# Kernel optimization log

Hardware: AMD Instinct MI355X
Metric: run time of the kernel (lower is better)

Reference implementation:

```python
import jax, jax.numpy as jnp
import numpy as np

# ---- constants mirroring the torch module's fixed config ----
H = W = 128            # raster_settings.image_size
K = 5                  # points_per_pixel
RADIUS = 0.02
R2 = RADIUS * RADIUS
DIST, ELEV = 1.5, 15.0 # look_at_view_transform(1.5, 15, views)
AZIMS = np.array([0.0, 90.0, 180.0, 270.0])
V = len(AZIMS)
ZNEAR, ZFAR = 0.01, 100.0  # FoVOrthographicCameras(znear=0.01), zfar default 100
N_PTS = 4096

def _look_at(dist, elev_deg, azims_deg):
    # pytorch3d camera_position_from_spherical_angles + look_at_rotation
    elev = np.deg2rad(elev_deg)
    az = np.deg2rad(azims_deg)
    C = np.stack([dist*np.cos(elev)*np.sin(az),
                  dist*np.sin(elev)*np.ones_like(az),
                  dist*np.cos(elev)*np.cos(az)], -1)            # [V,3] camera centers
    up = np.array([0.0, 1.0, 0.0])
    z_ax = -C / np.linalg.norm(C, axis=-1, keepdims=True)        # at=(0,0,0)
    x_ax = np.cross(np.broadcast_to(up, z_ax.shape), z_ax)
    x_ax = x_ax / np.linalg.norm(x_ax, axis=-1, keepdims=True)
    y_ax = np.cross(z_ax, x_ax)
    Rm = np.stack([x_ax, y_ax, z_ax], axis=-1)                   # columns = axes; X_view = X @ R + T
    T = -np.einsum('vji,vj->vi', Rm, C)
    return jnp.asarray(Rm, jnp.float32), jnp.asarray(T, jnp.float32)

_R, _T = _look_at(DIST, ELEV, AZIMS)

# pytorch3d NDC pixel centers (flipped: +X left, +Y up), flattened row-major p = yi*W + xi
_xf = 1.0 - (2.0*np.arange(W) + 1.0)/W
_yf = 1.0 - (2.0*np.arange(H) + 1.0)/H
XF = jnp.asarray(np.tile(_xf, H), jnp.float32)    # [H*W]
YF = jnp.asarray(np.repeat(_yf, W), jnp.float32)  # [H*W]


def _forward(pcd, displace, init_colors):
    colors_ = jax.nn.sigmoid(init_colors + displace)                 # [N]
    # world -> view -> NDC (orthographic: x,y pass through; z affine-normalized)
    pv = jnp.einsum('nj,vji->vni', pcd, _R) + _T[:, None, :]          # [V,N,3]
    px, py = pv[..., 0], pv[..., 1]
    pz = (pv[..., 2] - ZNEAR) / (ZFAR - ZNEAR)                        # [V,N]

    # ---- rasterization: per-pixel binning + depth top-K (non-differentiable selection) ----
    pxs, pys, pzs = map(jax.lax.stop_gradient, (px, py, pz))
    def sel(args):
        pxv, pyv, pzv = args                                          # [N] each
        dx = pxv[None, :] - XF[:, None]                               # [HW,N]
        dy = pyv[None, :] - YF[:, None]
        d2 = dx*dx + dy*dy
        score = jnp.where((d2 < R2) & (pzv[None, :] > 0), pzv[None, :], jnp.inf)
        negz, idx = jax.lax.top_k(-score, K)                          # nearest-z first
        return idx, negz
    idx, negz = jax.lax.map(sel, (pxs, pys, pzs))                     # [V,HW,K]
    valid = jnp.isfinite(negz)
    idxc = jnp.clip(idx, 0, pcd.shape[0] - 1)

    # differentiable re-gather of selected splats
    flat = idxc.reshape(V, -1)
    gpx = jnp.take_along_axis(px, flat, axis=1).reshape(idx.shape)    # [V,HW,K]
    gpy = jnp.take_along_axis(py, flat, axis=1).reshape(idx.shape)
    d2s = (gpx - XF[None, :, None])**2 + (gpy - YF[None, :, None])**2

    # ---- alpha compositing: w = 1 - d2/r^2, front-to-back over-composite, black bg ----
    alpha = jnp.where(valid, 1.0 - d2s / R2, 0.0)                     # [V,HW,K]
    feat = colors_[idxc]                                              # grayscale feature per splat
    t = jnp.cumprod(1.0 - alpha, axis=-1)
    t_excl = jnp.concatenate([jnp.ones_like(t[..., :1]), t[..., :-1]], -1)
    pix = jnp.sum(alpha * t_excl * feat, -1)                          # [V,HW]
    images = jnp.broadcast_to(pix[..., None], (V, H*W, 3)).reshape(V, H, W, 3)
    return images, colors_


def setup_inputs() -> dict:
    key = jax.random.key(0)
    k1, k2 = jax.random.split(key)
    pcd = jax.random.uniform(k1, (N_PTS, 3), jnp.float32) - 0.5
    displace = jax.random.normal(k2, (N_PTS,), jnp.float32) * 0.1
    init_colors = jnp.zeros((N_PTS,), jnp.float32)
    return {"pcd": pcd, "displace": displace, "init_colors": init_colors}


def reference(pcd, displace, init_colors):
    return _forward(pcd, displace, init_colors)
```

## Files before the change

kernel.cpp:

```cpp
#include <hip/hip_runtime.h>
#include <hip/hip_bf16.h>
#include <cmath>

#define NPTS  4096
#define HW    16384
#define WIDTH 128
#define NVIEW 4
#define KTOP  5
#define CAP   320

struct AllViews {
    float m[NVIEW][12];
};

__global__ __launch_bounds__(256, 4)
void raster_fused(const float* __restrict__ pcd,
                  const float* __restrict__ displace,
                  const float* __restrict__ init_colors,
                  float* __restrict__ out,
                  float* __restrict__ out_colors,
                  AllViews av) {
    __shared__ float4 buf[CAP];
    __shared__ int cnt;
    __shared__ float mzs[4][64][KTOP];
    __shared__ float mas[4][64][KTOP];
    __shared__ float mcs[4][64][KTOP];

    const int bid  = blockIdx.x;
    const int v    = bid >> 8;
    const int rem  = bid & 255;
    const int y    = rem >> 1;
    const int h    = rem & 1;
    const int tid  = threadIdx.x;
    const int wave = tid >> 6;
    const int lane = tid & 63;
    const float* M = av.m[v];

    if (tid == 0) cnt = 0;
    __syncthreads();

    const float4* __restrict__ pcd4 = (const float4*)pcd;
    const float4* __restrict__ d4   = (const float4*)displace;
    const float4* __restrict__ i4   = (const float4*)init_colors;

    #define PT(N, X0, X1, X2, SC)                                            \
    {                                                                        \
        float x0 = (X0), x1 = (X1), x2 = (X2);                               \
        float py = fmaf(x0, M[3], fmaf(x1, M[4], fmaf(x2, M[5], M[10])));    \
        int b = (int)floorf((1.0f - py) * 64.0f);                            \
        b = min(max(b, 0), 127);                                             \
        if ((b >= y - 1) & (b <= y + 1)) {                                   \
            float px  = fmaf(x0, M[0], fmaf(x1, M[1], fmaf(x2, M[2], M[9]))); \
            float pvz = fmaf(x0, M[6], fmaf(x1, M[7], fmaf(x2, M[8], M[11]))); \
            float pz  = (pvz - 0.01f) * (1.0f / 99.99f);                     \
            int pos = atomicAdd(&cnt, 1);                                    \
            if (pos < CAP) buf[pos] = make_float4(px, py, pz, (SC));         \
        }                                                                    \
        if ((v == 0) & (h == 0) & (((N) >> 5) == y)) out_colors[(N)] = (SC); \
    }

    #pragma unroll 1
    for (int ps = 0; ps < 4; ++ps) {
        float4 A = pcd4[ps * 768 + 3 * tid + 0];
        float4 B = pcd4[ps * 768 + 3 * tid + 1];
        float4 C = pcd4[ps * 768 + 3 * tid + 2];
        float4 D = d4[ps * 256 + tid];
        float4 I = i4[ps * 256 + tid];

        float4 S;
        S.x = 1.0f / (1.0f + expf(-(I.x + D.x)));
        S.y = 1.0f / (1.0f + expf(-(I.y + D.y)));
        S.z = 1.0f / (1.0f + expf(-(I.z + D.z)));
        S.w = 1.0f / (1.0f + expf(-(I.w + D.w)));

        const int n0 = (ps << 10) + (tid << 2);
        PT(n0 + 0, A.x, A.y, A.z, S.x);
        PT(n0 + 1, A.w, B.x, B.y, S.y);
        PT(n0 + 2, B.z, B.w, C.x, S.z);
        PT(n0 + 3, C.y, C.z, C.w, S.w);
    }
    #undef PT
    __syncthreads();

    const int m = min(cnt, CAP);

    const int xi = (h << 6) + lane;
    const float xf = 1.0f - (2.0f * (float)xi + 1.0f) * (1.0f / 128.0f);
    const float yf = 1.0f - (2.0f * (float)y + 1.0f) * (1.0f / 128.0f);

    const float R2f   = (float)(0.02 * 0.02);
    const float invR2 = 1.0f / R2f;

    #define INS(nz, na, nc)                                                 \
    {                                                                       \
        float _z = (nz), _a = (na), _c = (nc);                              \
        _Pragma("unroll")                                                   \
        for (int k = 0; k < KTOP; ++k) {                                    \
            bool sw = _z < zs[k];                                           \
            float oz = zs[k], oa = as_[k], oc = cs[k];                      \
            zs[k]  = sw ? _z : oz;                                          \
            as_[k] = sw ? _a : oa;                                          \
            cs[k]  = sw ? _c : oc;                                          \
            _z = sw ? oz : _z;                                              \
            _a = sw ? oa : _a;                                              \
            _c = sw ? oc : _c;                                              \
        }                                                                   \
    }

    float zs[KTOP], as_[KTOP], cs[KTOP];
    #pragma unroll
    for (int k = 0; k < KTOP; ++k) { zs[k] = 3.0e38f; as_[k] = 0.0f; cs[k] = 0.0f; }

    for (int j = wave; j < m; j += 4) {
        float4 pt = buf[j];
        float dx = pt.x - xf;
        float dy = pt.y - yf;
        float d2 = fmaf(dx, dx, dy * dy);
        if ((d2 < R2f) & (pt.z > 0.0f) & (pt.z < zs[KTOP - 1]))
            INS(pt.z, 1.0f - d2 * invR2, pt.w);
    }

    #pragma unroll
    for (int k = 0; k < KTOP; ++k) {
        mzs[wave][lane][k] = zs[k];
        mas[wave][lane][k] = as_[k];
        mcs[wave][lane][k] = cs[k];
    }
    __syncthreads();

    if (wave == 0) {
        #pragma unroll
        for (int k = 0; k < KTOP; ++k) { zs[k] = 3.0e38f; as_[k] = 0.0f; cs[k] = 0.0f; }
        #pragma unroll
        for (int w = 0; w < 4; ++w) {
            #pragma unroll
            for (int k = 0; k < KTOP; ++k) {
                float nz = mzs[w][lane][k];
                float na = mas[w][lane][k];
                float nc = mcs[w][lane][k];
                if (nz < zs[KTOP - 1]) INS(nz, na, nc);
            }
        }

        float t = 1.0f, pix = 0.0f;
        #pragma unroll
        for (int k = 0; k < KTOP; ++k) {
            pix += as_[k] * t * cs[k];
            t *= (1.0f - as_[k]);
        }

        const int p = v * HW + (y << 7) + xi;
        float* o = out + 3 * (size_t)p;
        o[0] = pix; o[1] = pix; o[2] = pix;
    }
    #undef INS
}

static void compute_views(AllViews* av) {
    const double dist = 1.5;
    const double elev = 15.0 * M_PI / 180.0;
    const double az_deg[NVIEW] = {0.0, 90.0, 180.0, 270.0};
    for (int v = 0; v < NVIEW; ++v) {
        double az = az_deg[v] * M_PI / 180.0;
        double C[3] = { dist * cos(elev) * sin(az),
                        dist * sin(elev),
                        dist * cos(elev) * cos(az) };
        double nC = sqrt(C[0]*C[0] + C[1]*C[1] + C[2]*C[2]);
        double z[3] = { -C[0]/nC, -C[1]/nC, -C[2]/nC };
        double up[3] = { 0.0, 1.0, 0.0 };
        double x[3] = { up[1]*z[2] - up[2]*z[1],
                        up[2]*z[0] - up[0]*z[2],
                        up[0]*z[1] - up[1]*z[0] };
        double nx = sqrt(x[0]*x[0] + x[1]*x[1] + x[2]*x[2]);
        x[0] /= nx; x[1] /= nx; x[2] /= nx;
        double y[3] = { z[1]*x[2] - z[2]*x[1],
                        z[2]*x[0] - z[0]*x[2],
                        z[0]*x[1] - z[1]*x[0] };
        double* axes[3] = { x, y, z };
        for (int i = 0; i < 3; ++i) {
            av->m[v][3*i + 0] = (float)axes[i][0];
            av->m[v][3*i + 1] = (float)axes[i][1];
            av->m[v][3*i + 2] = (float)axes[i][2];
            av->m[v][9 + i] = (float)(-(axes[i][0]*C[0] + axes[i][1]*C[1] + axes[i][2]*C[2]));
        }
    }
}

extern "C" void kernel_launch(void* const* d_in, const int* in_sizes, int n_in,
                              void* d_out, int out_size, void* d_ws, size_t ws_size,
                              hipStream_t stream) {
    const float* pcd         = (const float*)d_in[0];
    const float* displace    = (const float*)d_in[1];
    const float* init_colors = (const float*)d_in[2];
    float* out = (float*)d_out;
    float* out_colors = out + (size_t)NVIEW * HW * 3;

    AllViews av;
    compute_views(&av);

    raster_fused<<<NVIEW * 256, 256, 0, stream>>>(pcd, displace, init_colors,
                                                  out, out_colors, av);
}
```

Baseline: 79.65 us.

## Pre-bin projected points into per-view row buckets in a separate kernel

Splits the fused kernel into a memset, a prep kernel that projects every point once per view and scatters it into row buckets in the workspace, and a raster kernel that loads only its three neighbouring buckets. This removes the redundant work of each of the 1024 blocks reading and projecting all 4096 points. In exchange it adds two extra launches plus global atomics. Each bucket is capped at 160 points, so a dense row could overflow and drop points.

```diff
diff --git a/kernel.cpp b/kernel.cpp
--- a/kernel.cpp
+++ b/kernel.cpp
@@ -7,21 +7,52 @@
 #define WIDTH 128
 #define NVIEW 4
 #define KTOP  5
-#define CAP   320
+#define NBIN  128
+#define CAPB  160
 
 struct AllViews {
     float m[NVIEW][12];
 };
 
+#define WS_COUNTS  0
+#define WS_BUCKETS 2048
+
+__global__ __launch_bounds__(64)
+void prep_kernel(const float* __restrict__ pcd,
+                 const float* __restrict__ displace,
+                 const float* __restrict__ init_colors,
+                 float* __restrict__ out_colors,
+                 float4* __restrict__ buckets,
+                 int* __restrict__ counts,
+                 AllViews av) {
+    const int i = blockIdx.x * 64 + threadIdx.x;
+    const int v = i >> 12;
+    const int n = i & (NPTS - 1);
+    const float* M = av.m[v];
+
+    float p0 = pcd[3 * n + 0];
+    float p1 = pcd[3 * n + 1];
+    float p2 = pcd[3 * n + 2];
+    float px  = fmaf(p0, M[0], fmaf(p1, M[1], fmaf(p2, M[2], M[9])));
+    float py  = fmaf(p0, M[3], fmaf(p1, M[4], fmaf(p2, M[5], M[10])));
+    float pvz = fmaf(p0, M[6], fmaf(p1, M[7], fmaf(p2, M[8], M[11])));
+    float pz  = (pvz - 0.01f) * (1.0f / 99.99f);
+
+    float s = 1.0f / (1.0f + expf(-(init_colors[n] + displace[n])));
+    if (v == 0) out_colors[n] = s;
+
+    int b = (int)floorf((1.0f - py) * 64.0f);
+    b = min(max(b, 0), NBIN - 1);
+    int bk = (v << 7) + b;
+    int pos = atomicAdd(&counts[bk], 1);
+    if (pos < CAPB) buckets[(size_t)bk * CAPB + pos] = make_float4(px, py, pz, s);
+}
+
 __global__ __launch_bounds__(256, 4)
-void raster_fused(const float* __restrict__ pcd,
-                  const float* __restrict__ displace,
-                  const float* __restrict__ init_colors,
-                  float* __restrict__ out,
-                  float* __restrict__ out_colors,
-                  AllViews av) {
-    __shared__ float4 buf[CAP];
-    __shared__ int cnt;
+void raster_kernel(const float4* __restrict__ buckets,
+                   const int* __restrict__ counts,
+                   float* __restrict__ out) {
+    __shared__ float4 buf[3 * CAPB];
     __shared__ float mzs[4][64][KTOP];
     __shared__ float mas[4][64][KTOP];
     __shared__ float mcs[4][64][KTOP];
@@ -34,55 +65,28 @@
     const int tid  = threadIdx.x;
     const int wave = tid >> 6;
     const int lane = tid & 63;
-    const float* M = av.m[v];
-
-    if (tid == 0) cnt = 0;
+
+    const int b0 = max(y - 1, 0);
+    const int b1 = min(y + 1, NBIN - 1);
+
+    int c[3], off[4];
+    off[0] = 0;
+    #pragma unroll
+    for (int t = 0; t < 3; ++t) {
+        int b = b0 + t;
+        int cc = (b <= b1) ? min(counts[(v << 7) + b], CAPB) : 0;
+        c[t] = cc;
+        off[t + 1] = off[t] + cc;
+    }
+
+    #pragma unroll
+    for (int t = 0; t < 3; ++t) {
+        if (tid < c[t])
+            buf[off[t] + tid] = buckets[((size_t)((v << 7) + b0 + t)) * CAPB + tid];
+    }
     __syncthreads();
 
-    const float4* __restrict__ pcd4 = (const float4*)pcd;
-    const float4* __restrict__ d4   = (const float4*)displace;
-    const float4* __restrict__ i4   = (const float4*)init_colors;
-
-    #define PT(N, X0, X1, X2, SC)                                            \
-    {                                                                        \
-        float x0 = (X0), x1 = (X1), x2 = (X2);                               \
-        float py = fmaf(x0, M[3], fmaf(x1, M[4], fmaf(x2, M[5], M[10])));    \
-        int b = (int)floorf((1.0f - py) * 64.0f);                            \
-        b = min(max(b, 0), 127);                                             \
-        if ((b >= y - 1) & (b <= y + 1)) {                                   \
-            float px  = fmaf(x0, M[0], fmaf(x1, M[1], fmaf(x2, M[2], M[9]))); \
-            float pvz = fmaf(x0, M[6], fmaf(x1, M[7], fmaf(x2, M[8], M[11]))); \
-            float pz  = (pvz - 0.01f) * (1.0f / 99.99f);                     \
-            int pos = atomicAdd(&cnt, 1);                                    \
-            if (pos < CAP) buf[pos] = make_float4(px, py, pz, (SC));         \
-        }                                                                    \
-        if ((v == 0) & (h == 0) & (((N) >> 5) == y)) out_colors[(N)] = (SC); \
-    }
-
-    #pragma unroll 1
-    for (int ps = 0; ps < 4; ++ps) {
-        float4 A = pcd4[ps * 768 + 3 * tid + 0];
-        float4 B = pcd4[ps * 768 + 3 * tid + 1];
-        float4 C = pcd4[ps * 768 + 3 * tid + 2];
-        float4 D = d4[ps * 256 + tid];
-        float4 I = i4[ps * 256 + tid];
-
-        float4 S;
-        S.x = 1.0f / (1.0f + expf(-(I.x + D.x)));
-        S.y = 1.0f / (1.0f + expf(-(I.y + D.y)));
-        S.z = 1.0f / (1.0f + expf(-(I.z + D.z)));
-        S.w = 1.0f / (1.0f + expf(-(I.w + D.w)));
-
-        const int n0 = (ps << 10) + (tid << 2);
-        PT(n0 + 0, A.x, A.y, A.z, S.x);
-        PT(n0 + 1, A.w, B.x, B.y, S.y);
-        PT(n0 + 2, B.z, B.w, C.x, S.z);
-        PT(n0 + 3, C.y, C.z, C.w, S.w);
-    }
-    #undef PT
-    __syncthreads();
-
-    const int m = min(cnt, CAP);
+    const int m = off[3];
 
     const int xi = (h << 6) + lane;
     const float xf = 1.0f - (2.0f * (float)xi + 1.0f) * (1.0f / 128.0f);
@@ -136,9 +140,7 @@
             #pragma unroll
             for (int k = 0; k < KTOP; ++k) {
                 float nz = mzs[w][lane][k];
-                float na = mas[w][lane][k];
-                float nc = mcs[w][lane][k];
-                if (nz < zs[KTOP - 1]) INS(nz, na, nc);
+                if (nz < zs[KTOP - 1]) INS(nz, mas[w][lane][k], mcs[w][lane][k]);
             }
         }
 
@@ -195,9 +197,15 @@
     float* out = (float*)d_out;
     float* out_colors = out + (size_t)NVIEW * HW * 3;
 
+    char* ws = (char*)d_ws;
+    int* counts     = (int*)(ws + WS_COUNTS);
+    float4* buckets = (float4*)(ws + WS_BUCKETS);
+
     AllViews av;
     compute_views(&av);
 
-    raster_fused<<<NVIEW * 256, 256, 0, stream>>>(pcd, displace, init_colors,
-                                                  out, out_colors, av);
-}
+    hipMemsetAsync(counts, 0, NVIEW * NBIN * sizeof(int), stream);
+    prep_kernel<<<NVIEW * NPTS / 64, 64, 0, stream>>>(pcd, displace, init_colors,
+                                                      out_colors, buckets, counts, av);
+    raster_kernel<<<NVIEW * 256, 256, 0, stream>>>(buckets, counts, out);
+}
```

Result: no change. 79.54 us (-0.1%).
